# Optimization experiments

Measured on AMD Instinct MI355X. Metric: run time of the kernel, lower is better.

Reference implementation:

```python
import jax, jax.numpy as jnp
import numpy as np

NUM_HEADS = 32
NUM_KV_HEADS = 8
HEAD_DIM = 128
SCALE = 1.0 / np.sqrt(HEAD_DIM)
BATCH = 16
MAX_CTX = 2048
NUM_SLOTS = BATCH * MAX_CTX + BATCH  # 32784; last BATCH slots are the write targets


def setup_inputs() -> dict:
    key = jax.random.key(0)
    ks = jax.random.split(key, 8)
    q = jax.random.normal(ks[0], (BATCH, NUM_HEADS, HEAD_DIM), dtype=jnp.float32)
    k = jax.random.normal(ks[1], (BATCH, NUM_KV_HEADS, HEAD_DIM), dtype=jnp.float32)
    v = jax.random.normal(ks[2], (BATCH, NUM_KV_HEADS, HEAD_DIM), dtype=jnp.float32)
    k_cache = jax.random.normal(ks[3], (NUM_SLOTS, NUM_KV_HEADS, HEAD_DIM), dtype=jnp.float32)
    v_cache = jax.random.normal(ks[4], (NUM_SLOTS, NUM_KV_HEADS, HEAD_DIM), dtype=jnp.float32)
    # each decode token writes its new kv into a fresh slot at the end of the pool
    slot_mapping = (BATCH * MAX_CTX + jnp.arange(BATCH)).astype(jnp.int64)
    # sparse-controller-selected active slots per request (paged, irregular)
    active_slots = jax.random.randint(ks[5], (BATCH, MAX_CTX), 0, NUM_SLOTS).astype(jnp.int64)
    # make the current token's slot the last active slot of its own request
    active_slots = active_slots.at[:, -1].set(slot_mapping)
    context_lens = jax.random.randint(ks[6], (BATCH,), 1, MAX_CTX + 1).astype(jnp.int64)
    return {
        "q": q, "k": k, "v": v,
        "k_cache": k_cache, "v_cache": v_cache,
        "slot_mapping": slot_mapping,
        "active_slots": active_slots,
        "context_lens": context_lens,
    }


def _attend(q, k, v, k_cache, v_cache, slot_mapping, active_slots, context_lens):
    # store_kvcache: scatter new k/v into flat slot cache; slot == -1 is skipped
    safe_slots = jnp.where(slot_mapping < 0, NUM_SLOTS, slot_mapping)  # OOB -> dropped
    kc = k_cache.at[safe_slots].set(k, mode="drop")
    vc = v_cache.at[safe_slots].set(v, mode="drop")

    # paged gather of the per-request active KV pages
    K = kc[active_slots]  # [B, L, Hkv, D]
    V = vc[active_slots]  # [B, L, Hkv, D]

    B, H, D = q.shape
    G = H // NUM_KV_HEADS  # GQA group size
    qg = q.reshape(B, NUM_KV_HEADS, G, D)

    # flash-decode stage1+stage2 == numerically-stable softmax attention over active slots
    scores = jnp.einsum("bkgd,blkd->bkgl", qg, K) * SCALE  # [B, Hkv, G, L]
    valid = jnp.arange(active_slots.shape[1])[None, :] < context_lens[:, None]  # [B, L]
    scores = jnp.where(valid[:, None, None, :], scores, jnp.float32(-1e30))
    p = jax.nn.softmax(scores, axis=-1)
    o = jnp.einsum("bkgl,blkd->bkgd", p, V).reshape(B, H, D)
    return o


def reference(q, k, v, k_cache, v_cache, slot_mapping, active_slots, context_lens):
    return _attend(q, k, v, k_cache, v_cache, slot_mapping, active_slots, context_lens)
```

## Files before the change

### kernel.cpp

```cpp
#include <hip/hip_runtime.h>
#include <hip/hip_bf16.h>
#include <float.h>

#define B 16
#define H 32
#define HKV 8
#define G 4
#define D 128
#define LMAX 2048
#define BATCH 32
#define SCALE 0.08838834764831844f

__device__ __forceinline__ void stage16(const float* gsrc, float* lds_base, int lane) {
#if __has_builtin(__builtin_amdgcn_global_load_lds)
    __builtin_amdgcn_global_load_lds(
        (const __attribute__((address_space(1))) void*)gsrc,
        (__attribute__((address_space(3))) void*)lds_base, 16, 0, 0);
#else
    *(float4*)((char*)lds_base + lane * 16) = *(const float4*)gsrc;
#endif
}

template <int CHUNK>
__global__ __launch_bounds__(256) void attn_partial(
    const float* __restrict__ q,
    const float* __restrict__ kin,
    const float* __restrict__ vin,
    const float* __restrict__ kc,
    const float* __restrict__ vc,
    const int*  __restrict__ slot_mapping,
    const int*  __restrict__ active_slots,
    const int*  __restrict__ context_lens,
    float* __restrict__ part_o,
    float* __restrict__ part_ml)
{
    constexpr int NSPLIT = LMAX / CHUNK;
    const int tid   = threadIdx.x;
    const int split = blockIdx.x % NSPLIT;
    const int h     = (blockIdx.x / NSPLIT) % HKV;
    const int b     = blockIdx.x / (NSPLIT * HKV);

    const int ctx   = context_lens[b];
    const int start = split * CHUNK;
    int nvalid = ctx - start;
    if (nvalid > CHUNK) nvalid = CHUNK;

    const size_t pbase = ((size_t)(b * HKV + h) * NSPLIT + split) * G;

    if (nvalid <= 0) {
        if (tid < G * 2) part_ml[pbase * 2 + tid] = (tid & 1) ? 0.f : -FLT_MAX;
        return;
    }

    __shared__ float stg[2][BATCH * D];
    __shared__ float sc[CHUNK][G];
    __shared__ const float* kp[CHUNK];
    __shared__ const float* vp[CHUNK];
    __shared__ int sm[16];

    if (tid < 16) sm[tid] = slot_mapping[tid];
    __syncthreads();

    for (int li = tid; li < nvalid; li += 256) {
        const int s = active_slots[b * LMAX + start + li];
        int ov = -1;
#pragma unroll
        for (int j = 0; j < 16; ++j)
            if (sm[j] == s) ov = j;
        kp[li] = (ov >= 0) ? kin + ((size_t)ov * HKV + h) * D : kc + ((size_t)s * HKV + h) * D;
        vp[li] = (ov >= 0) ? vin + ((size_t)ov * HKV + h) * D : vc + ((size_t)s * HKV + h) * D;
    }

    const int grp   = tid >> 3;
    const int lane8 = tid & 7;
    const int wv    = tid >> 6;
    const int lane  = tid & 63;

    float4 qv[G][4];
#pragma unroll
    for (int g = 0; g < G; ++g) {
        const float* qp = q + ((size_t)(b * H + h * G + g)) * D;
#pragma unroll
        for (int i = 0; i < 4; ++i) {
            float4 t = *(const float4*)(qp + i * 32 + lane8 * 4);
            qv[g][i] = make_float4(t.x * SCALE, t.y * SCALE, t.z * SCALE, t.w * SCALE);
        }
    }
    __syncthreads();

    const int nb = (nvalid + BATCH - 1) / BATCH;

    auto STAGE = [&](const float* const* ptrs, int t, int buf) {
#pragma unroll
        for (int p = 0; p < 4; ++p) {
            const int r  = wv * 8 + 2 * p + (lane >> 5);
            const int li = t * BATCH + r;
            if (li < nvalid)
                stage16(ptrs[li] + (lane & 31) * 4, &stg[buf][(wv * 8 + 2 * p) * D], lane);
        }
    };

    auto COMPUTE_QK = [&](int t, int buf) {
        const int li = t * BATCH + grp;
        if (li < nvalid) {
            const float* kr = &stg[buf][grp * D];
            float pd0 = 0.f, pd1 = 0.f, pd2 = 0.f, pd3 = 0.f;
#pragma unroll
            for (int j = 0; j < 4; ++j) {
                const float4 kv = *(const float4*)(kr + j * 32 + lane8 * 4);
                pd0 += kv.x * qv[0][j].x + kv.y * qv[0][j].y + kv.z * qv[0][j].z + kv.w * qv[0][j].w;
                pd1 += kv.x * qv[1][j].x + kv.y * qv[1][j].y + kv.z * qv[1][j].z + kv.w * qv[1][j].w;
                pd2 += kv.x * qv[2][j].x + kv.y * qv[2][j].y + kv.z * qv[2][j].z + kv.w * qv[2][j].w;
                pd3 += kv.x * qv[3][j].x + kv.y * qv[3][j].y + kv.z * qv[3][j].z + kv.w * qv[3][j].w;
            }
#pragma unroll
            for (int msk = 1; msk < 8; msk <<= 1) {
                pd0 += __shfl_xor(pd0, msk, 8);
                pd1 += __shfl_xor(pd1, msk, 8);
                pd2 += __shfl_xor(pd2, msk, 8);
                pd3 += __shfl_xor(pd3, msk, 8);
            }
            if (lane8 == 0)
                *(float4*)&sc[li][0] = make_float4(pd0, pd1, pd2, pd3);
        }
    };

    STAGE(kp, 0, 0);
    __syncthreads();
    for (int t = 0; t < nb; ++t) {
        if (t + 1 < nb) STAGE(kp, t + 1, (t + 1) & 1);
        else            STAGE(vp, 0, nb & 1);
        COMPUTE_QK(t, t & 1);
        __syncthreads();
    }

    {
        const int g = wv;
        float m = -FLT_MAX;
        for (int i = lane; i < nvalid; i += 64) m = fmaxf(m, sc[i][g]);
#pragma unroll
        for (int msk = 1; msk < 64; msk <<= 1) m = fmaxf(m, __shfl_xor(m, msk, 64));
        float sum = 0.f;
        for (int i = lane; i < nvalid; i += 64) {
            const float p = __expf(sc[i][g] - m);
            sc[i][g] = p;
            sum += p;
        }
#pragma unroll
        for (int msk = 1; msk < 64; msk <<= 1) sum += __shfl_xor(sum, msk, 64);
        if (lane == 0) {
            part_ml[(pbase + g) * 2 + 0] = m;
            part_ml[(pbase + g) * 2 + 1] = sum;
        }
    }
    __syncthreads();

    const int grp8 = tid >> 5;
    const int dl   = tid & 31;
    float4 a0 = {0,0,0,0}, a1 = {0,0,0,0}, a2 = {0,0,0,0}, a3 = {0,0,0,0};
    for (int t = 0; t < nb; ++t) {
        if (t + 1 < nb) STAGE(vp, t + 1, (nb + t + 1) & 1);
        const int buf = (nb + t) & 1;
#pragma unroll
        for (int ii = 0; ii < 4; ++ii) {
            const int r  = ii * 8 + grp8;
            const int li = t * BATCH + r;
            if (li < nvalid) {
                const float4 vv = *(const float4*)(&stg[buf][r * D + dl * 4]);
                const float4 p4 = *(const float4*)&sc[li][0];
                a0.x += p4.x * vv.x; a0.y += p4.x * vv.y; a0.z += p4.x * vv.z; a0.w += p4.x * vv.w;
                a1.x += p4.y * vv.x; a1.y += p4.y * vv.y; a1.z += p4.y * vv.z; a1.w += p4.y * vv.w;
                a2.x += p4.z * vv.x; a2.y += p4.z * vv.y; a2.z += p4.z * vv.z; a2.w += p4.z * vv.w;
                a3.x += p4.w * vv.x; a3.y += p4.w * vv.y; a3.z += p4.w * vv.z; a3.w += p4.w * vv.w;
            }
        }
        __syncthreads();
    }

    {
        float* red = &stg[0][0];
        *(float4*)&red[((grp8 * G + 0) * D) + dl * 4] = a0;
        *(float4*)&red[((grp8 * G + 1) * D) + dl * 4] = a1;
        *(float4*)&red[((grp8 * G + 2) * D) + dl * 4] = a2;
        *(float4*)&red[((grp8 * G + 3) * D) + dl * 4] = a3;
        __syncthreads();
#pragma unroll
        for (int k2 = 0; k2 < 2; ++k2) {
            const int o = tid * 2 + k2;
            const int g = o >> 7, d = o & 127;
            float s = 0.f;
#pragma unroll
            for (int r = 0; r < 8; ++r) s += red[(r * G + g) * D + d];
            part_o[(pbase + g) * D + d] = s;
        }
    }
}

__global__ __launch_bounds__(128) void attn_reduce(
    const float* __restrict__ part_o,
    const float* __restrict__ part_ml,
    float* __restrict__ out,
    int nsplit)
{
    const int g = blockIdx.x & 3;
    const int h = (blockIdx.x >> 2) & 7;
    const int b = blockIdx.x >> 5;
    const int d = threadIdx.x;

    __shared__ float mlds[32], llds[32];
    const size_t base = (size_t)(b * HKV + h) * nsplit;

    for (int s = d; s < nsplit; s += 128) {
        mlds[s] = part_ml[((base + s) * G + g) * 2 + 0];
        llds[s] = part_ml[((base + s) * G + g) * 2 + 1];
    }
    __syncthreads();

    float M = -FLT_MAX;
    for (int s = 0; s < nsplit; ++s)
        if (llds[s] > 0.f) M = fmaxf(M, mlds[s]);

    float L = 0.f, acc = 0.f;
    for (int s = 0; s < nsplit; ++s) {
        const float l = llds[s];
        if (l > 0.f) {
            const float e = __expf(mlds[s] - M);
            L += l * e;
            acc += e * part_o[((base + s) * G + g) * D + d];
        }
    }
    out[((size_t)(b * H) + h * G + g) * D + d] = acc / (L > 0.f ? L : 1.f);
}

extern "C" void kernel_launch(void* const* d_in, const int* in_sizes, int n_in,
                              void* d_out, int out_size, void* d_ws, size_t ws_size,
                              hipStream_t stream) {
    const float* q  = (const float*)d_in[0];
    const float* k  = (const float*)d_in[1];
    const float* v  = (const float*)d_in[2];
    const float* kc = (const float*)d_in[3];
    const float* vc = (const float*)d_in[4];
    const int* slot_mapping = (const int*)d_in[5];
    const int* active_slots = (const int*)d_in[6];
    const int* context_lens = (const int*)d_in[7];
    float* out = (float*)d_out;

    const size_t perSplit = (size_t)B * HKV * (G * D + G * 2) * sizeof(float);
    const int nsplit = (ws_size >= 16 * perSplit) ? 16 : 8;

    float* part_o  = (float*)d_ws;
    float* part_ml = part_o + (size_t)B * HKV * nsplit * G * D;

    if (nsplit == 16) {
        attn_partial<128><<<B * HKV * 16, 256, 0, stream>>>(
            q, k, v, kc, vc, slot_mapping, active_slots, context_lens, part_o, part_ml);
    } else {
        attn_partial<256><<<B * HKV * 8, 256, 0, stream>>>(
            q, k, v, kc, vc, slot_mapping, active_slots, context_lens, part_o, part_ml);
    }
    attn_reduce<<<B * HKV * G, 128, 0, stream>>>(part_o, part_ml, out, nsplit);
}
```

Measured before the change: 43.01 us.

## Unify K/V staging into one pipelined loop with swizzled LDS layout

New measurement: 62.05 us. 44.3% more time.

```diff
diff --git a/kernel.cpp b/kernel.cpp
--- a/kernel.cpp
+++ b/kernel.cpp
@@ -11,12 +11,13 @@
 #define BATCH 32
 #define SCALE 0.08838834764831844f
 
-__device__ __forceinline__ void stage16(const float* gsrc, float* lds_base, int lane) {
+__device__ __forceinline__ void stage16(const float* gsrc, float* lds_base) {
 #if __has_builtin(__builtin_amdgcn_global_load_lds)
     __builtin_amdgcn_global_load_lds(
         (const __attribute__((address_space(1))) void*)gsrc,
         (__attribute__((address_space(3))) void*)lds_base, 16, 0, 0);
 #else
+    const int lane = threadIdx.x & 63;
     *(float4*)((char*)lds_base + lane * 16) = *(const float4*)gsrc;
 #endif
 }
@@ -75,6 +76,8 @@
     const int lane8 = tid & 7;
     const int wv    = tid >> 6;
     const int lane  = tid & 63;
+    const int grp8  = tid >> 5;
+    const int dl    = tid & 31;
 
     float4 qv[G][4];
 #pragma unroll
@@ -89,25 +92,31 @@
     __syncthreads();
 
     const int nb = (nvalid + BATCH - 1) / BATCH;
-
-    auto STAGE = [&](const float* const* ptrs, int t, int buf) {
+    const int NT = 2 * nb;
+
+    auto STAGE = [&](int st) {
+        const float* const* ptrs = (st < nb) ? kp : vp;
+        const int tb = (st < nb) ? st : st - nb;
 #pragma unroll
         for (int p = 0; p < 4; ++p) {
             const int r  = wv * 8 + 2 * p + (lane >> 5);
-            const int li = t * BATCH + r;
-            if (li < nvalid)
-                stage16(ptrs[li] + (lane & 31) * 4, &stg[buf][(wv * 8 + 2 * p) * D], lane);
+            int li = tb * BATCH + r;
+            if (li >= nvalid) li = nvalid - 1;
+            stage16(ptrs[li] + (((lane & 31) ^ (r & 7)) * 4),
+                    &stg[st & 1][(wv * 8 + 2 * p) * D]);
         }
     };
 
-    auto COMPUTE_QK = [&](int t, int buf) {
+    auto COMPUTE_QK = [&](int t) {
         const int li = t * BATCH + grp;
         if (li < nvalid) {
-            const float* kr = &stg[buf][grp * D];
+            const float* kr = &stg[t & 1][grp * D];
+            const int sw = grp & 7;
             float pd0 = 0.f, pd1 = 0.f, pd2 = 0.f, pd3 = 0.f;
 #pragma unroll
             for (int j = 0; j < 4; ++j) {
-                const float4 kv = *(const float4*)(kr + j * 32 + lane8 * 4);
+                const int slot = (j * 8 + lane8) ^ sw;
+                const float4 kv = *(const float4*)(kr + slot * 4);
                 pd0 += kv.x * qv[0][j].x + kv.y * qv[0][j].y + kv.z * qv[0][j].z + kv.w * qv[0][j].w;
                 pd1 += kv.x * qv[1][j].x + kv.y * qv[1][j].y + kv.z * qv[1][j].z + kv.w * qv[1][j].w;
                 pd2 += kv.x * qv[2][j].x + kv.y * qv[2][j].y + kv.z * qv[2][j].z + kv.w * qv[2][j].w;
@@ -125,48 +134,15 @@
         }
     };
 
-    STAGE(kp, 0, 0);
-    __syncthreads();
-    for (int t = 0; t < nb; ++t) {
-        if (t + 1 < nb) STAGE(kp, t + 1, (t + 1) & 1);
-        else            STAGE(vp, 0, nb & 1);
-        COMPUTE_QK(t, t & 1);
-        __syncthreads();
-    }
-
-    {
-        const int g = wv;
-        float m = -FLT_MAX;
-        for (int i = lane; i < nvalid; i += 64) m = fmaxf(m, sc[i][g]);
-#pragma unroll
-        for (int msk = 1; msk < 64; msk <<= 1) m = fmaxf(m, __shfl_xor(m, msk, 64));
-        float sum = 0.f;
-        for (int i = lane; i < nvalid; i += 64) {
-            const float p = __expf(sc[i][g] - m);
-            sc[i][g] = p;
-            sum += p;
-        }
-#pragma unroll
-        for (int msk = 1; msk < 64; msk <<= 1) sum += __shfl_xor(sum, msk, 64);
-        if (lane == 0) {
-            part_ml[(pbase + g) * 2 + 0] = m;
-            part_ml[(pbase + g) * 2 + 1] = sum;
-        }
-    }
-    __syncthreads();
-
-    const int grp8 = tid >> 5;
-    const int dl   = tid & 31;
     float4 a0 = {0,0,0,0}, a1 = {0,0,0,0}, a2 = {0,0,0,0}, a3 = {0,0,0,0};
-    for (int t = 0; t < nb; ++t) {
-        if (t + 1 < nb) STAGE(vp, t + 1, (nb + t + 1) & 1);
-        const int buf = (nb + t) & 1;
+    auto COMPUTE_PV = [&](int tv) {
+        const int buf = (nb + tv) & 1;
 #pragma unroll
         for (int ii = 0; ii < 4; ++ii) {
             const int r  = ii * 8 + grp8;
-            const int li = t * BATCH + r;
+            const int li = tv * BATCH + r;
             if (li < nvalid) {
-                const float4 vv = *(const float4*)(&stg[buf][r * D + dl * 4]);
+                const float4 vv = *(const float4*)(&stg[buf][r * D + ((dl ^ (r & 7)) * 4)]);
                 const float4 p4 = *(const float4*)&sc[li][0];
                 a0.x += p4.x * vv.x; a0.y += p4.x * vv.y; a0.z += p4.x * vv.z; a0.w += p4.x * vv.w;
                 a1.x += p4.y * vv.x; a1.y += p4.y * vv.y; a1.z += p4.y * vv.z; a1.w += p4.y * vv.w;
@@ -174,9 +150,44 @@
                 a3.x += p4.w * vv.x; a3.y += p4.w * vv.y; a3.z += p4.w * vv.z; a3.w += p4.w * vv.w;
             }
         }
-        __syncthreads();
-    }
-
+    };
+
+    STAGE(0);
+    if (NT > 1) STAGE(1);
+    for (int t = 0; t < NT; ++t) {
+        if (t < NT - 1) asm volatile("s_waitcnt vmcnt(4)" ::: "memory");
+        else            asm volatile("s_waitcnt vmcnt(0)" ::: "memory");
+        __builtin_amdgcn_s_barrier();
+
+        if (t == nb) {
+            const int g = wv;
+            float m = -FLT_MAX;
+            for (int i = lane; i < nvalid; i += 64) m = fmaxf(m, sc[i][g]);
+#pragma unroll
+            for (int msk = 1; msk < 64; msk <<= 1) m = fmaxf(m, __shfl_xor(m, msk, 64));
+            float sum = 0.f;
+            for (int i = lane; i < nvalid; i += 64) {
+                const float p = __expf(sc[i][g] - m);
+                sc[i][g] = p;
+                sum += p;
+            }
+#pragma unroll
+            for (int msk = 1; msk < 64; msk <<= 1) sum += __shfl_xor(sum, msk, 64);
+            if (lane == 0) {
+                part_ml[(pbase + g) * 2 + 0] = m;
+                part_ml[(pbase + g) * 2 + 1] = sum;
+            }
+            __builtin_amdgcn_s_barrier();
+        }
+
+        if (t < nb) COMPUTE_QK(t);
+        else        COMPUTE_PV(t - nb);
+
+        __builtin_amdgcn_s_barrier();
+        if (t + 2 < NT) STAGE(t + 2);
+    }
+
+    __syncthreads();
     {
         float* red = &stg[0][0];
         *(float4*)&red[((grp8 * G + 0) * D) + dl * 4] = a0;
```

## Use single-wave blocks with direct global loads and finer context splits

Applied to the files above, without the earlier changes.

New measurement: 41.82 us, median of 2. -2.8%, faster.

```diff
diff --git a/kernel.cpp b/kernel.cpp
--- a/kernel.cpp
+++ b/kernel.cpp
@@ -8,21 +8,10 @@
 #define G 4
 #define D 128
 #define LMAX 2048
-#define BATCH 32
 #define SCALE 0.08838834764831844f
 
-__device__ __forceinline__ void stage16(const float* gsrc, float* lds_base, int lane) {
-#if __has_builtin(__builtin_amdgcn_global_load_lds)
-    __builtin_amdgcn_global_load_lds(
-        (const __attribute__((address_space(1))) void*)gsrc,
-        (__attribute__((address_space(3))) void*)lds_base, 16, 0, 0);
-#else
-    *(float4*)((char*)lds_base + lane * 16) = *(const float4*)gsrc;
-#endif
-}
-
 template <int CHUNK>
-__global__ __launch_bounds__(256) void attn_partial(
+__global__ __launch_bounds__(64, 3) void attn_partial(
     const float* __restrict__ q,
     const float* __restrict__ kin,
     const float* __restrict__ vin,
@@ -52,29 +41,22 @@
         return;
     }
 
-    __shared__ float stg[2][BATCH * D];
-    __shared__ float sc[CHUNK][G];
     __shared__ const float* kp[CHUNK];
     __shared__ const float* vp[CHUNK];
-    __shared__ int sm[16];
-
-    if (tid < 16) sm[tid] = slot_mapping[tid];
-    __syncthreads();
-
-    for (int li = tid; li < nvalid; li += 256) {
+    __shared__ float4 sc4[CHUNK];
+
+    for (int li = tid; li < nvalid; li += 64) {
         const int s = active_slots[b * LMAX + start + li];
         int ov = -1;
 #pragma unroll
         for (int j = 0; j < 16; ++j)
-            if (sm[j] == s) ov = j;
+            if (slot_mapping[j] == s) ov = j;
         kp[li] = (ov >= 0) ? kin + ((size_t)ov * HKV + h) * D : kc + ((size_t)s * HKV + h) * D;
         vp[li] = (ov >= 0) ? vin + ((size_t)ov * HKV + h) * D : vc + ((size_t)s * HKV + h) * D;
     }
 
     const int grp   = tid >> 3;
     const int lane8 = tid & 7;
-    const int wv    = tid >> 6;
-    const int lane  = tid & 63;
 
     float4 qv[G][4];
 #pragma unroll
@@ -86,112 +68,104 @@
             qv[g][i] = make_float4(t.x * SCALE, t.y * SCALE, t.z * SCALE, t.w * SCALE);
         }
     }
-    __syncthreads();
-
-    const int nb = (nvalid + BATCH - 1) / BATCH;
-
-    auto STAGE = [&](const float* const* ptrs, int t, int buf) {
-#pragma unroll
-        for (int p = 0; p < 4; ++p) {
-            const int r  = wv * 8 + 2 * p + (lane >> 5);
-            const int li = t * BATCH + r;
-            if (li < nvalid)
-                stage16(ptrs[li] + (lane & 31) * 4, &stg[buf][(wv * 8 + 2 * p) * D], lane);
-        }
-    };
-
-    auto COMPUTE_QK = [&](int t, int buf) {
-        const int li = t * BATCH + grp;
-        if (li < nvalid) {
-            const float* kr = &stg[buf][grp * D];
-            float pd0 = 0.f, pd1 = 0.f, pd2 = 0.f, pd3 = 0.f;
-#pragma unroll
-            for (int j = 0; j < 4; ++j) {
-                const float4 kv = *(const float4*)(kr + j * 32 + lane8 * 4);
-                pd0 += kv.x * qv[0][j].x + kv.y * qv[0][j].y + kv.z * qv[0][j].z + kv.w * qv[0][j].w;
-                pd1 += kv.x * qv[1][j].x + kv.y * qv[1][j].y + kv.z * qv[1][j].z + kv.w * qv[1][j].w;
-                pd2 += kv.x * qv[2][j].x + kv.y * qv[2][j].y + kv.z * qv[2][j].z + kv.w * qv[2][j].w;
-                pd3 += kv.x * qv[3][j].x + kv.y * qv[3][j].y + kv.z * qv[3][j].z + kv.w * qv[3][j].w;
-            }
-#pragma unroll
-            for (int msk = 1; msk < 8; msk <<= 1) {
-                pd0 += __shfl_xor(pd0, msk, 8);
-                pd1 += __shfl_xor(pd1, msk, 8);
-                pd2 += __shfl_xor(pd2, msk, 8);
-                pd3 += __shfl_xor(pd3, msk, 8);
-            }
-            if (lane8 == 0)
-                *(float4*)&sc[li][0] = make_float4(pd0, pd1, pd2, pd3);
-        }
-    };
-
-    STAGE(kp, 0, 0);
-    __syncthreads();
-    for (int t = 0; t < nb; ++t) {
-        if (t + 1 < nb) STAGE(kp, t + 1, (t + 1) & 1);
-        else            STAGE(vp, 0, nb & 1);
-        COMPUTE_QK(t, t & 1);
-        __syncthreads();
+
+    constexpr int KIT = CHUNK / 8;
+#pragma unroll 2
+    for (int it = 0; it < KIT; ++it) {
+        const int r  = it * 8 + grp;
+        const int rl = (r < nvalid) ? r : nvalid - 1;
+        const float* kb = kp[rl];
+        float pd0 = 0.f, pd1 = 0.f, pd2 = 0.f, pd3 = 0.f;
+#pragma unroll
+        for (int j = 0; j < 4; ++j) {
+            const float4 kv = *(const float4*)(kb + j * 32 + lane8 * 4);
+            pd0 += kv.x * qv[0][j].x + kv.y * qv[0][j].y + kv.z * qv[0][j].z + kv.w * qv[0][j].w;
+            pd1 += kv.x * qv[1][j].x + kv.y * qv[1][j].y + kv.z * qv[1][j].z + kv.w * qv[1][j].w;
+            pd2 += kv.x * qv[2][j].x + kv.y * qv[2][j].y + kv.z * qv[2][j].z + kv.w * qv[2][j].w;
+            pd3 += kv.x * qv[3][j].x + kv.y * qv[3][j].y + kv.z * qv[3][j].z + kv.w * qv[3][j].w;
+        }
+#pragma unroll
+        for (int msk = 1; msk < 8; msk <<= 1) {
+            pd0 += __shfl_xor(pd0, msk, 8);
+            pd1 += __shfl_xor(pd1, msk, 8);
+            pd2 += __shfl_xor(pd2, msk, 8);
+            pd3 += __shfl_xor(pd3, msk, 8);
+        }
+        if (lane8 == 0) sc4[r] = make_float4(pd0, pd1, pd2, pd3);
     }
 
     {
-        const int g = wv;
-        float m = -FLT_MAX;
-        for (int i = lane; i < nvalid; i += 64) m = fmaxf(m, sc[i][g]);
-#pragma unroll
-        for (int msk = 1; msk < 64; msk <<= 1) m = fmaxf(m, __shfl_xor(m, msk, 64));
-        float sum = 0.f;
-        for (int i = lane; i < nvalid; i += 64) {
-            const float p = __expf(sc[i][g] - m);
-            sc[i][g] = p;
-            sum += p;
-        }
-#pragma unroll
-        for (int msk = 1; msk < 64; msk <<= 1) sum += __shfl_xor(sum, msk, 64);
-        if (lane == 0) {
-            part_ml[(pbase + g) * 2 + 0] = m;
-            part_ml[(pbase + g) * 2 + 1] = sum;
-        }
-    }
-    __syncthreads();
-
-    const int grp8 = tid >> 5;
-    const int dl   = tid & 31;
-    float4 a0 = {0,0,0,0}, a1 = {0,0,0,0}, a2 = {0,0,0,0}, a3 = {0,0,0,0};
-    for (int t = 0; t < nb; ++t) {
-        if (t + 1 < nb) STAGE(vp, t + 1, (nb + t + 1) & 1);
-        const int buf = (nb + t) & 1;
-#pragma unroll
-        for (int ii = 0; ii < 4; ++ii) {
-            const int r  = ii * 8 + grp8;
-            const int li = t * BATCH + r;
-            if (li < nvalid) {
-                const float4 vv = *(const float4*)(&stg[buf][r * D + dl * 4]);
-                const float4 p4 = *(const float4*)&sc[li][0];
-                a0.x += p4.x * vv.x; a0.y += p4.x * vv.y; a0.z += p4.x * vv.z; a0.w += p4.x * vv.w;
-                a1.x += p4.y * vv.x; a1.y += p4.y * vv.y; a1.z += p4.y * vv.z; a1.w += p4.y * vv.w;
-                a2.x += p4.z * vv.x; a2.y += p4.z * vv.y; a2.z += p4.z * vv.z; a2.w += p4.z * vv.w;
-                a3.x += p4.w * vv.x; a3.y += p4.w * vv.y; a3.z += p4.w * vv.z; a3.w += p4.w * vv.w;
-            }
-        }
-        __syncthreads();
+        constexpr int SR = (CHUNK + 63) / 64;
+        float4 s[SR];
+#pragma unroll
+        for (int k2 = 0; k2 < SR; ++k2) {
+            const int l = tid + k2 * 64;
+            s[k2] = sc4[l];
+            if (l >= nvalid) s[k2] = make_float4(-1e30f, -1e30f, -1e30f, -1e30f);
+        }
+        float m0 = s[0].x, m1 = s[0].y, m2 = s[0].z, m3 = s[0].w;
+#pragma unroll
+        for (int k2 = 1; k2 < SR; ++k2) {
+            m0 = fmaxf(m0, s[k2].x); m1 = fmaxf(m1, s[k2].y);
+            m2 = fmaxf(m2, s[k2].z); m3 = fmaxf(m3, s[k2].w);
+        }
+#pragma unroll
+        for (int msk = 1; msk < 64; msk <<= 1) {
+            m0 = fmaxf(m0, __shfl_xor(m0, msk));
+            m1 = fmaxf(m1, __shfl_xor(m1, msk));
+            m2 = fmaxf(m2, __shfl_xor(m2, msk));
+            m3 = fmaxf(m3, __shfl_xor(m3, msk));
+        }
+        float l0 = 0.f, l1 = 0.f, l2 = 0.f, l3 = 0.f;
+#pragma unroll
+        for (int k2 = 0; k2 < SR; ++k2) {
+            const float4 p = make_float4(__expf(s[k2].x - m0), __expf(s[k2].y - m1),
+                                         __expf(s[k2].z - m2), __expf(s[k2].w - m3));
+            l0 += p.x; l1 += p.y; l2 += p.z; l3 += p.w;
+            sc4[tid + k2 * 64] = p;
+        }
+#pragma unroll
+        for (int msk = 1; msk < 64; msk <<= 1) {
+            l0 += __shfl_xor(l0, msk);
+            l1 += __shfl_xor(l1, msk);
+            l2 += __shfl_xor(l2, msk);
+            l3 += __shfl_xor(l3, msk);
+        }
+        if (tid == 0) {
+            *(float4*)&part_ml[pbase * 2 + 0] = make_float4(m0, l0, m1, l1);
+            *(float4*)&part_ml[pbase * 2 + 4] = make_float4(m2, l2, m3, l3);
+        }
     }
 
     {
-        float* red = &stg[0][0];
-        *(float4*)&red[((grp8 * G + 0) * D) + dl * 4] = a0;
-        *(float4*)&red[((grp8 * G + 1) * D) + dl * 4] = a1;
-        *(float4*)&red[((grp8 * G + 2) * D) + dl * 4] = a2;
-        *(float4*)&red[((grp8 * G + 3) * D) + dl * 4] = a3;
-        __syncthreads();
-#pragma unroll
-        for (int k2 = 0; k2 < 2; ++k2) {
-            const int o = tid * 2 + k2;
-            const int g = o >> 7, d = o & 127;
-            float s = 0.f;
-#pragma unroll
-            for (int r = 0; r < 8; ++r) s += red[(r * G + g) * D + d];
-            part_o[(pbase + g) * D + d] = s;
+        const int half = tid >> 5;
+        const int dl   = tid & 31;
+        float4 a0 = {0,0,0,0}, a1 = {0,0,0,0}, a2 = {0,0,0,0}, a3 = {0,0,0,0};
+        constexpr int VJ = CHUNK / 2;
+#pragma unroll 4
+        for (int j = 0; j < VJ; ++j) {
+            const int r  = 2 * j + half;
+            const int rl = (r < nvalid) ? r : nvalid - 1;
+            const float4 vv = *(const float4*)(vp[rl] + dl * 4);
+            const float4 p4 = sc4[r];
+            a0.x += p4.x * vv.x; a0.y += p4.x * vv.y; a0.z += p4.x * vv.z; a0.w += p4.x * vv.w;
+            a1.x += p4.y * vv.x; a1.y += p4.y * vv.y; a1.z += p4.y * vv.z; a1.w += p4.y * vv.w;
+            a2.x += p4.z * vv.x; a2.y += p4.z * vv.y; a2.z += p4.z * vv.z; a2.w += p4.z * vv.w;
+            a3.x += p4.w * vv.x; a3.y += p4.w * vv.y; a3.z += p4.w * vv.z; a3.w += p4.w * vv.w;
+        }
+#pragma unroll
+        for (int c = 0; c < 4; ++c) {
+            ((float*)&a0)[c] += __shfl_xor(((float*)&a0)[c], 32);
+            ((float*)&a1)[c] += __shfl_xor(((float*)&a1)[c], 32);
+            ((float*)&a2)[c] += __shfl_xor(((float*)&a2)[c], 32);
+            ((float*)&a3)[c] += __shfl_xor(((float*)&a3)[c], 32);
+        }
+        if (half == 0) {
+            *(float4*)(part_o + (pbase + 0) * D + dl * 4) = a0;
+            *(float4*)(part_o + (pbase + 1) * D + dl * 4) = a1;
+        } else {
+            *(float4*)(part_o + (pbase + 2) * D + dl * 4) = a2;
+            *(float4*)(part_o + (pbase + 3) * D + dl * 4) = a3;
         }
     }
 }
@@ -246,16 +220,21 @@
     float* out = (float*)d_out;
 
     const size_t perSplit = (size_t)B * HKV * (G * D + G * 2) * sizeof(float);
-    const int nsplit = (ws_size >= 16 * perSplit) ? 16 : 8;
+    int nsplit = 8;
+    if (ws_size >= 32 * perSplit)      nsplit = 32;
+    else if (ws_size >= 16 * perSplit) nsplit = 16;
 
     float* part_o  = (float*)d_ws;
     float* part_ml = part_o + (size_t)B * HKV * nsplit * G * D;
 
-    if (nsplit == 16) {
-        attn_partial<128><<<B * HKV * 16, 256, 0, stream>>>(
+    if (nsplit == 32) {
+        attn_partial<64><<<B * HKV * 32, 64, 0, stream>>>(
+            q, k, v, kc, vc, slot_mapping, active_slots, context_lens, part_o, part_ml);
+    } else if (nsplit == 16) {
+        attn_partial<128><<<B * HKV * 16, 64, 0, stream>>>(
             q, k, v, kc, vc, slot_mapping, active_slots, context_lens, part_o, part_ml);
     } else {
-        attn_partial<256><<<B * HKV * 8, 256, 0, stream>>>(
+        attn_partial<256><<<B * HKV * 8, 64, 0, stream>>>(
             q, k, v, kc, vc, slot_mapping, active_slots, context_lens, part_o, part_ml);
     }
     attn_reduce<<<B * HKV * G, 128, 0, stream>>>(part_o, part_ml, out, nsplit);
```
